# Optimization experiments

Measured on AMD Instinct MI355X. Metric: run time of the kernel, lower is better.

## Reference

```python
import jax, jax.numpy as jnp
import numpy as np

NUM_ENTITIES = 500000
NUM_RELATIONS = 100
DIM = 64
BATCH = 4096
N_MEM = 256


def setup_inputs() -> dict:
    key = jax.random.key(0)
    ks = jax.random.split(key, 12)
    # xavier_uniform bound for [N, D]: sqrt(6/(N+D))
    def xavier(k, shape):
        bound = np.sqrt(6.0 / (shape[0] + shape[1]))
        return jax.random.uniform(k, shape, jnp.float32, -bound, bound)
    inp = {
        "item_ids": jax.random.randint(ks[0], (BATCH,), 0, NUM_ENTITIES),
        "hop0_h": jax.random.randint(ks[1], (BATCH, N_MEM), 0, NUM_ENTITIES),
        "hop0_r": jax.random.randint(ks[2], (BATCH, N_MEM), 0, NUM_RELATIONS),
        "hop0_t": jax.random.randint(ks[3], (BATCH, N_MEM), 0, NUM_ENTITIES),
        "hop1_h": jax.random.randint(ks[4], (BATCH, N_MEM), 0, NUM_ENTITIES),
        "hop1_r": jax.random.randint(ks[5], (BATCH, N_MEM), 0, NUM_RELATIONS),
        "hop1_t": jax.random.randint(ks[6], (BATCH, N_MEM), 0, NUM_ENTITIES),
        "entity_emb": xavier(ks[7], (NUM_ENTITIES, DIM)),
        "relation_emb": xavier(ks[8], (NUM_RELATIONS, DIM)),
        "W0": xavier(ks[9], (DIM, DIM)),  # nn.Linear weight [out, in]
        "W1": xavier(ks[10], (DIM, DIM)),
    }
    return inp


def _hop(item_emb, h_idx, r_idx, t_idx, entity_emb, relation_emb, W):
    h = entity_emb[h_idx]          # [B, M, D]
    r = relation_emb[r_idx]        # [B, M, D]
    t = entity_emb[t_idx]          # [B, M, D]
    hr = h * r
    attn = jax.nn.softmax(jnp.einsum("bmd,bd->bm", hr, item_emb), axis=-1)
    o = jnp.einsum("bm,bmd->bd", attn, t)
    return (item_emb + o) @ W.T    # Linear(bias=False): x @ W^T


def reference(item_ids, hop0_h, hop0_r, hop0_t, hop1_h, hop1_r, hop1_t,
              entity_emb, relation_emb, W0, W1):
    item_emb = entity_emb[item_ids]  # [B, D]
    item_emb = _hop(item_emb, hop0_h, hop0_r, hop0_t, entity_emb, relation_emb, W0)
    item_emb = _hop(item_emb, hop1_h, hop1_r, hop1_t, entity_emb, relation_emb, W1)
    return item_emb.sum(axis=-1)     # [B]
```

## Files before the change

### kernel.cpp

```cpp
#include <hip/hip_runtime.h>

#define NMEM 256
#define DIM  64


__global__ __launch_bounds__(256, 4)
void ripplenet_kernel(const int* __restrict__ item_ids,
                      const int* __restrict__ h0, const int* __restrict__ r0, const int* __restrict__ t0,
                      const int* __restrict__ h1, const int* __restrict__ r1, const int* __restrict__ t1,
                      const float* __restrict__ ent, const float* __restrict__ rel,
                      const float* __restrict__ W0, const float* __restrict__ W1,
                      float* __restrict__ out)
{
    __shared__ float4 sRedO[64];
    __shared__ float4 sRedY[64];
    __shared__ float  sSm[4];

    const int tid  = threadIdx.x;
    const int lane = tid & 63;
    const int wave = tid >> 6;
    const int g    = lane >> 4;
    const int l16  = lane & 15;
    const int b    = blockIdx.x;

    const float4* ent4 = (const float4*)ent;
    const float4* rel4 = (const float4*)rel;

    const int base = b * NMEM + wave * 64 + lane;
    const int ihA = h0[base], irA = r0[base], itA = t0[base];
    const int ihB = h1[base], irB = r1[base], itB = t1[base];

    float4 xv = ent4[item_ids[b] * 16 + l16];

    for (int hop = 0; hop < 2; ++hop) {
        const int ih = hop ? ihB : ihA;
        const int ir = hop ? irB : irA;
        const int it = hop ? itB : itA;
        const float4* W4 = (const float4*)(hop ? W1 : W0);

        float4 acc = {0.f, 0.f, 0.f, 0.f};
        float  sm  = 0.f;

        #pragma unroll 8
        for (int i = 0; i < 16; ++i) {
            int j   = i * 4 + g;
            int ihj = __shfl(ih, j, 64);
            int irj = __shfl(ir, j, 64);
            int itj = __shfl(it, j, 64);
            float4 hv = ent4[ihj * 16 + l16];
            float4 rv = rel4[irj * 16 + l16];
            float4 tv = ent4[itj * 16 + l16];
            float v = hv.x*rv.x*xv.x + hv.y*rv.y*xv.y + hv.z*rv.z*xv.z + hv.w*rv.w*xv.w;
            v += __shfl_xor(v, 1, 64);
            v += __shfl_xor(v, 2, 64);
            v += __shfl_xor(v, 4, 64);
            v += __shfl_xor(v, 8, 64);
            float p = __expf(v);
            sm    += p;
            acc.x += p * tv.x; acc.y += p * tv.y;
            acc.z += p * tv.z; acc.w += p * tv.w;
        }

        acc.x += __shfl_xor(acc.x, 16, 64); acc.y += __shfl_xor(acc.y, 16, 64);
        acc.z += __shfl_xor(acc.z, 16, 64); acc.w += __shfl_xor(acc.w, 16, 64);
        acc.x += __shfl_xor(acc.x, 32, 64); acc.y += __shfl_xor(acc.y, 32, 64);
        acc.z += __shfl_xor(acc.z, 32, 64); acc.w += __shfl_xor(acc.w, 32, 64);
        sm += __shfl_xor(sm, 16, 64);
        sm += __shfl_xor(sm, 32, 64);

        if (lane < 16) sRedO[wave * 16 + lane] = acc;
        if (lane == 0) sSm[wave] = sm;
        __syncthreads();

        float smt = sSm[0] + sSm[1] + sSm[2] + sSm[3];
        float inv = 1.0f / smt;
        float4 o0 = sRedO[l16],      o1 = sRedO[16 + l16];
        float4 o2 = sRedO[32 + l16], o3 = sRedO[48 + l16];
        float4 xo;
        xo.x = xv.x + (o0.x + o1.x + o2.x + o3.x) * inv;
        xo.y = xv.y + (o0.y + o1.y + o2.y + o3.y) * inv;
        xo.z = xv.z + (o0.z + o1.z + o2.z + o3.z) * inv;
        xo.w = xv.w + (o0.w + o1.w + o2.w + o3.w) * inv;

        int k = wave * 4 + g;
        float xod0 = __shfl(xo.x, k, 64);
        float xod1 = __shfl(xo.y, k, 64);
        float xod2 = __shfl(xo.z, k, 64);
        float xod3 = __shfl(xo.w, k, 64);
        float4 w0 = W4[(l16 * 4 + 0) * 16 + k];
        float4 w1 = W4[(l16 * 4 + 1) * 16 + k];
        float4 w2 = W4[(l16 * 4 + 2) * 16 + k];
        float4 w3 = W4[(l16 * 4 + 3) * 16 + k];
        float4 y;
        y.x = xod0*w0.x + xod1*w0.y + xod2*w0.z + xod3*w0.w;
        y.y = xod0*w1.x + xod1*w1.y + xod2*w1.z + xod3*w1.w;
        y.z = xod0*w2.x + xod1*w2.y + xod2*w2.z + xod3*w2.w;
        y.w = xod0*w3.x + xod1*w3.y + xod2*w3.z + xod3*w3.w;

        y.x += __shfl_xor(y.x, 16, 64); y.y += __shfl_xor(y.y, 16, 64);
        y.z += __shfl_xor(y.z, 16, 64); y.w += __shfl_xor(y.w, 16, 64);
        y.x += __shfl_xor(y.x, 32, 64); y.y += __shfl_xor(y.y, 32, 64);
        y.z += __shfl_xor(y.z, 32, 64); y.w += __shfl_xor(y.w, 32, 64);

        if (lane < 16) sRedY[wave * 16 + lane] = y;
        __syncthreads();

        float4 y0 = sRedY[l16],      y1 = sRedY[16 + l16];
        float4 y2 = sRedY[32 + l16], y3 = sRedY[48 + l16];
        xv.x = y0.x + y1.x + y2.x + y3.x;
        xv.y = y0.y + y1.y + y2.y + y3.y;
        xv.z = y0.z + y1.z + y2.z + y3.z;
        xv.w = y0.w + y1.w + y2.w + y3.w;
    }

    if (wave == 0) {
        float s = xv.x + xv.y + xv.z + xv.w;
        s += __shfl_xor(s, 1, 64);
        s += __shfl_xor(s, 2, 64);
        s += __shfl_xor(s, 4, 64);
        s += __shfl_xor(s, 8, 64);
        if (lane == 0) out[b] = s;
    }
}

extern "C" void kernel_launch(void* const* d_in, const int* in_sizes, int n_in,
                              void* d_out, int out_size, void* d_ws, size_t ws_size,
                              hipStream_t stream) {
    const int*   item_ids = (const int*)  d_in[0];
    const int*   h0       = (const int*)  d_in[1];
    const int*   r0       = (const int*)  d_in[2];
    const int*   t0       = (const int*)  d_in[3];
    const int*   h1       = (const int*)  d_in[4];
    const int*   r1       = (const int*)  d_in[5];
    const int*   t1       = (const int*)  d_in[6];
    const float* ent      = (const float*)d_in[7];
    const float* rel      = (const float*)d_in[8];
    const float* W0       = (const float*)d_in[9];
    const float* W1       = (const float*)d_in[10];
    float* out = (float*)d_out;

    ripplenet_kernel<<<4096, 256, 0, stream>>>(item_ids, h0, r0, t0, h1, r1, t1,
                                               ent, rel, W0, W1, out);
}
```

Measured before the change: 325.0 us.

## Convert embedding tables to bf16 each call and gather half-width rows

```diff
diff --git a/kernel.cpp b/kernel.cpp
--- a/kernel.cpp
+++ b/kernel.cpp
@@ -3,14 +3,174 @@
 #define NMEM 256
 #define DIM  64
 
+__device__ __forceinline__ unsigned pack_bf2(float a, float b) {
+    unsigned ua = __float_as_uint(a), ub = __float_as_uint(b);
+    ua += 0x7FFFu + ((ua >> 16) & 1u);
+    ub += 0x7FFFu + ((ub >> 16) & 1u);
+    return (ua >> 16) | (ub & 0xFFFF0000u);
+}
+__device__ __forceinline__ float bflo(unsigned u) { return __uint_as_float(u << 16); }
+__device__ __forceinline__ float bfhi(unsigned u) { return __uint_as_float(u & 0xFFFF0000u); }
+
+__global__ __launch_bounds__(256)
+void cvt_kernel(const float4* __restrict__ src, uint4* __restrict__ dst, int n8) {
+    int i = blockIdx.x * 256 + threadIdx.x;
+    if (i < n8) {
+        float4 a = src[2 * i], b = src[2 * i + 1];
+        uint4 o;
+        o.x = pack_bf2(a.x, a.y); o.y = pack_bf2(a.z, a.w);
+        o.z = pack_bf2(b.x, b.y); o.w = pack_bf2(b.z, b.w);
+        dst[i] = o;
+    }
+}
 
 __global__ __launch_bounds__(256, 4)
-void ripplenet_kernel(const int* __restrict__ item_ids,
-                      const int* __restrict__ h0, const int* __restrict__ r0, const int* __restrict__ t0,
-                      const int* __restrict__ h1, const int* __restrict__ r1, const int* __restrict__ t1,
-                      const float* __restrict__ ent, const float* __restrict__ rel,
-                      const float* __restrict__ W0, const float* __restrict__ W1,
-                      float* __restrict__ out)
+void ripplenet_bf16_kernel(const int* __restrict__ item_ids,
+                           const int* __restrict__ h0, const int* __restrict__ r0, const int* __restrict__ t0,
+                           const int* __restrict__ h1, const int* __restrict__ r1, const int* __restrict__ t1,
+                           const float* __restrict__ ent, const float* __restrict__ W0,
+                           const float* __restrict__ W1,
+                           const uint4* __restrict__ entB, const uint4* __restrict__ relB,
+                           float* __restrict__ out)
+{
+    __shared__ float4 sRedO[64];
+    __shared__ float4 sRedY[64];
+    __shared__ float  sSm[4];
+
+    const int tid  = threadIdx.x;
+    const int lane = tid & 63;
+    const int wave = tid >> 6;
+    const int g    = lane >> 4;
+    const int l16  = lane & 15;
+    const int g8   = lane >> 3;
+    const int l8   = lane & 7;
+    const int b    = blockIdx.x;
+
+    const float4* ent4 = (const float4*)ent;
+
+    const int base = b * NMEM + wave * 64 + lane;
+    const int ihA = h0[base], irA = r0[base], itA = t0[base];
+    const int ihB = h1[base], irB = r1[base], itB = t1[base];
+
+    const int id = item_ids[b];
+    float4 xa = ent4[id * 16 + 2 * l8];
+    float4 xb = ent4[id * 16 + 2 * l8 + 1];
+    float4 xv = ent4[id * 16 + l16];
+
+    for (int hop = 0; hop < 2; ++hop) {
+        const int ih = hop ? ihB : ihA;
+        const int ir = hop ? irB : irA;
+        const int it = hop ? itB : itA;
+        const float4* W4 = (const float4*)(hop ? W1 : W0);
+
+        float4 accA = {0.f,0.f,0.f,0.f}, accB = {0.f,0.f,0.f,0.f};
+        float  sm   = 0.f;
+
+        #pragma unroll 4
+        for (int i = 0; i < 8; ++i) {
+            int j   = i * 8 + g8;
+            int ihj = __shfl(ih, j, 64);
+            int irj = __shfl(ir, j, 64);
+            int itj = __shfl(it, j, 64);
+            uint4 hv = entB[ihj * 8 + l8];
+            uint4 rv = relB[irj * 8 + l8];
+            uint4 tv = entB[itj * 8 + l8];
+            float v = bflo(hv.x)*bflo(rv.x)*xa.x + bfhi(hv.x)*bfhi(rv.x)*xa.y
+                    + bflo(hv.y)*bflo(rv.y)*xa.z + bfhi(hv.y)*bfhi(rv.y)*xa.w
+                    + bflo(hv.z)*bflo(rv.z)*xb.x + bfhi(hv.z)*bfhi(rv.z)*xb.y
+                    + bflo(hv.w)*bflo(rv.w)*xb.z + bfhi(hv.w)*bfhi(rv.w)*xb.w;
+            v += __shfl_xor(v, 1, 64);
+            v += __shfl_xor(v, 2, 64);
+            v += __shfl_xor(v, 4, 64);
+            float p = __expf(v);
+            sm += p;
+            accA.x += p * bflo(tv.x); accA.y += p * bfhi(tv.x);
+            accA.z += p * bflo(tv.y); accA.w += p * bfhi(tv.y);
+            accB.x += p * bflo(tv.z); accB.y += p * bfhi(tv.z);
+            accB.z += p * bflo(tv.w); accB.w += p * bfhi(tv.w);
+        }
+
+        #pragma unroll
+        for (int off = 8; off <= 32; off <<= 1) {
+            accA.x += __shfl_xor(accA.x, off, 64); accA.y += __shfl_xor(accA.y, off, 64);
+            accA.z += __shfl_xor(accA.z, off, 64); accA.w += __shfl_xor(accA.w, off, 64);
+            accB.x += __shfl_xor(accB.x, off, 64); accB.y += __shfl_xor(accB.y, off, 64);
+            accB.z += __shfl_xor(accB.z, off, 64); accB.w += __shfl_xor(accB.w, off, 64);
+            sm     += __shfl_xor(sm,     off, 64);
+        }
+
+        if (lane < 8) {
+            sRedO[wave * 16 + 2 * l8]     = accA;
+            sRedO[wave * 16 + 2 * l8 + 1] = accB;
+        }
+        if (lane == 0) sSm[wave] = sm;
+        __syncthreads();
+
+        float smt = sSm[0] + sSm[1] + sSm[2] + sSm[3];
+        float inv = 1.0f / smt;
+        float4 o0 = sRedO[l16],      o1 = sRedO[16 + l16];
+        float4 o2 = sRedO[32 + l16], o3 = sRedO[48 + l16];
+        float4 xo;
+        xo.x = xv.x + (o0.x + o1.x + o2.x + o3.x) * inv;
+        xo.y = xv.y + (o0.y + o1.y + o2.y + o3.y) * inv;
+        xo.z = xv.z + (o0.z + o1.z + o2.z + o3.z) * inv;
+        xo.w = xv.w + (o0.w + o1.w + o2.w + o3.w) * inv;
+
+        int k = wave * 4 + g;
+        float xod0 = __shfl(xo.x, k, 64);
+        float xod1 = __shfl(xo.y, k, 64);
+        float xod2 = __shfl(xo.z, k, 64);
+        float xod3 = __shfl(xo.w, k, 64);
+        float4 w0 = W4[(l16 * 4 + 0) * 16 + k];
+        float4 w1 = W4[(l16 * 4 + 1) * 16 + k];
+        float4 w2 = W4[(l16 * 4 + 2) * 16 + k];
+        float4 w3 = W4[(l16 * 4 + 3) * 16 + k];
+        float4 y;
+        y.x = xod0*w0.x + xod1*w0.y + xod2*w0.z + xod3*w0.w;
+        y.y = xod0*w1.x + xod1*w1.y + xod2*w1.z + xod3*w1.w;
+        y.z = xod0*w2.x + xod1*w2.y + xod2*w2.z + xod3*w2.w;
+        y.w = xod0*w3.x + xod1*w3.y + xod2*w3.z + xod3*w3.w;
+
+        y.x += __shfl_xor(y.x, 16, 64); y.y += __shfl_xor(y.y, 16, 64);
+        y.z += __shfl_xor(y.z, 16, 64); y.w += __shfl_xor(y.w, 16, 64);
+        y.x += __shfl_xor(y.x, 32, 64); y.y += __shfl_xor(y.y, 32, 64);
+        y.z += __shfl_xor(y.z, 32, 64); y.w += __shfl_xor(y.w, 32, 64);
+
+        if (lane < 16) sRedY[wave * 16 + lane] = y;
+        __syncthreads();
+
+        float4 y0 = sRedY[l16],      y1 = sRedY[16 + l16];
+        float4 y2 = sRedY[32 + l16], y3 = sRedY[48 + l16];
+        xv.x = y0.x + y1.x + y2.x + y3.x;
+        xv.y = y0.y + y1.y + y2.y + y3.y;
+        xv.z = y0.z + y1.z + y2.z + y3.z;
+        xv.w = y0.w + y1.w + y2.w + y3.w;
+
+        if (hop == 0) {
+            xa.x = __shfl(xv.x, 2*l8,     64); xa.y = __shfl(xv.y, 2*l8,     64);
+            xa.z = __shfl(xv.z, 2*l8,     64); xa.w = __shfl(xv.w, 2*l8,     64);
+            xb.x = __shfl(xv.x, 2*l8 + 1, 64); xb.y = __shfl(xv.y, 2*l8 + 1, 64);
+            xb.z = __shfl(xv.z, 2*l8 + 1, 64); xb.w = __shfl(xv.w, 2*l8 + 1, 64);
+        }
+    }
+
+    if (wave == 0) {
+        float s = xv.x + xv.y + xv.z + xv.w;
+        s += __shfl_xor(s, 1, 64);
+        s += __shfl_xor(s, 2, 64);
+        s += __shfl_xor(s, 4, 64);
+        s += __shfl_xor(s, 8, 64);
+        if (lane == 0) out[b] = s;
+    }
+}
+
+__global__ __launch_bounds__(256, 4)
+void ripplenet_f32_kernel(const int* __restrict__ item_ids,
+                          const int* __restrict__ h0, const int* __restrict__ r0, const int* __restrict__ t0,
+                          const int* __restrict__ h1, const int* __restrict__ r1, const int* __restrict__ t1,
+                          const float* __restrict__ ent, const float* __restrict__ rel,
+                          const float* __restrict__ W0, const float* __restrict__ W1,
+                          float* __restrict__ out)
 {
     __shared__ float4 sRedO[64];
     __shared__ float4 sRedY[64];
@@ -41,7 +201,7 @@
         float4 acc = {0.f, 0.f, 0.f, 0.f};
         float  sm  = 0.f;
 
-        #pragma unroll 8
+        #pragma unroll 4
         for (int i = 0; i < 16; ++i) {
             int j   = i * 4 + g;
             int ihj = __shfl(ih, j, 64);
@@ -139,6 +299,19 @@
     const float* W1       = (const float*)d_in[10];
     float* out = (float*)d_out;
 
-    ripplenet_kernel<<<4096, 256, 0, stream>>>(item_ids, h0, r0, t0, h1, r1, t1,
-                                               ent, rel, W0, W1, out);
-}
+    const size_t entBytesB = (size_t)500000 * 64 * 2;
+    const size_t relBytesB = (size_t)100 * 64 * 2;
+    if (ws_size >= entBytesB + relBytesB) {
+        uint4* entB = (uint4*)d_ws;
+        uint4* relB = (uint4*)((char*)d_ws + entBytesB);
+        int entN8 = 500000 * 64 / 8;
+        int relN8 = 100 * 64 / 8;
+        cvt_kernel<<<(entN8 + 255) / 256, 256, 0, stream>>>((const float4*)ent, entB, entN8);
+        cvt_kernel<<<(relN8 + 255) / 256, 256, 0, stream>>>((const float4*)rel, relB, relN8);
+        ripplenet_bf16_kernel<<<4096, 256, 0, stream>>>(item_ids, h0, r0, t0, h1, r1, t1,
+                                                        ent, W0, W1, entB, relB, out);
+    } else {
+        ripplenet_f32_kernel<<<4096, 256, 0, stream>>>(item_ids, h0, r0, t0, h1, r1, t1,
+                                                       ent, rel, W0, W1, out);
+    }
+}
```

Result: faster. 296.4 us, median of 2 (-8.8%).
